# Optimization experiments

Measured on AMD Instinct MI355X. Metric: run time of the kernel, lower is better.

Reference implementation:

```python
import jax, jax.numpy as jnp
import numpy as np

H = 200          # GRU hidden size (hard-coded in module)
D = 300          # embed_dim
V = 50000        # embed_num (vocab)
DOC_TRUNC = 10
N_DOCS = 256
T = 50           # words per sentence


def _p(k, shape):
    return jax.random.normal(k, shape, dtype=jnp.float32) * 0.05


def setup_inputs():
    key = jax.random.key(0)
    ks = jax.random.split(key, 24)
    x = jax.random.randint(ks[0], (N_DOCS * DOC_TRUNC, T), 0, V, dtype=jnp.int32)
    doc_lens = jax.random.randint(ks[1], (N_DOCS,), 0, DOC_TRUNC + 1, dtype=jnp.int32)
    emb = _p(ks[2], (V, D)).at[0].set(0.0)  # padding_idx=0 row is zero
    inp = dict(
        x=x, doc_nums=N_DOCS, doc_lens=doc_lens, emb=emb,
        wf_ih=_p(ks[3], (3 * H, D)), wf_hh=_p(ks[4], (3 * H, H)), wf_bi=_p(ks[5], (3 * H,)), wf_bh=_p(ks[6], (3 * H,)),
        wb_ih=_p(ks[7], (3 * H, D)), wb_hh=_p(ks[8], (3 * H, H)), wb_bi=_p(ks[9], (3 * H,)), wb_bh=_p(ks[10], (3 * H,)),
        sf_ih=_p(ks[11], (3 * H, 2 * H)), sf_hh=_p(ks[12], (3 * H, H)), sf_bi=_p(ks[13], (3 * H,)), sf_bh=_p(ks[14], (3 * H,)),
        sb_ih=_p(ks[15], (3 * H, 2 * H)), sb_hh=_p(ks[16], (3 * H, H)), sb_bi=_p(ks[17], (3 * H,)), sb_bh=_p(ks[18], (3 * H,)),
        doc_w=_p(ks[19], (1, 2 * H)), doc_b=_p(ks[20], (1,)),
        sent_w=_p(ks[21], (DOC_TRUNC, 2 * H)), sent_b=_p(ks[22], (DOC_TRUNC,)),
    )
    return inp


def _gru_dir(xseq, w_ih, w_hh, b_ih, b_hh, reverse=False):
    # xseq: [B, T, Din] -> outputs [B, T, H], torch GRU gate order (r, z, n)
    if reverse:
        xseq = xseq[:, ::-1]
    gx = jnp.einsum('btd,gd->btg', xseq, w_ih) + b_ih  # [B, T, 3H]
    gx = jnp.moveaxis(gx, 1, 0)                        # [T, B, 3H]
    h0 = jnp.zeros((xseq.shape[0], H), xseq.dtype)

    def step(h, gxt):
        gh = h @ w_hh.T + b_hh
        xr, xz, xn = jnp.split(gxt, 3, axis=-1)
        hr, hz, hn = jnp.split(gh, 3, axis=-1)
        r = jax.nn.sigmoid(xr + hr)
        z = jax.nn.sigmoid(xz + hz)
        n = jnp.tanh(xn + r * hn)
        h_new = (1.0 - z) * n + z * h
        return h_new, h_new

    _, hs = jax.lax.scan(step, h0, gx)
    hs = jnp.moveaxis(hs, 0, 1)  # [B, T, H]
    if reverse:
        hs = hs[:, ::-1]
    return hs


def _bigru(xseq, fw, bw):
    return jnp.concatenate([_gru_dir(xseq, *fw), _gru_dir(xseq, *bw, reverse=True)], axis=-1)


def _avg_pool(xseq, lens):
    # Faithful to max_pool1d helper: avg over first lens[i] timesteps, zeros if len==0.
    Tn = xseq.shape[1]
    mask = (jnp.arange(Tn)[None, :] < lens[:, None]).astype(xseq.dtype)  # [B, T]
    s = jnp.einsum('btf,bt->bf', xseq, mask)
    denom = jnp.maximum(lens, 1).astype(xseq.dtype)[:, None]
    return jnp.where((lens == 0)[:, None], jnp.zeros_like(s), s / denom)


def reference(x, doc_nums, doc_lens, emb,
              wf_ih, wf_hh, wf_bi, wf_bh, wb_ih, wb_hh, wb_bi, wb_bh,
              sf_ih, sf_hh, sf_bi, sf_bh, sb_ih, sb_hh, sb_bi, sb_bh,
              doc_w, doc_b, sent_w, sent_b):
    sent_lens = jnp.sum(jnp.sign(x), axis=1)                 # [B_sent]
    e = emb[x]                                               # [B_sent, T, D]
    hw = _bigru(e, (wf_ih, wf_hh, wf_bi, wf_bh), (wb_ih, wb_hh, wb_bi, wb_bh))  # [B_sent, T, 2H]
    s = _avg_pool(hw, sent_lens)                             # [B_sent, 2H]
    s = s.reshape(-1, DOC_TRUNC, 2 * H)                      # [N_docs, doc_trunc, 2H]
    hs = _bigru(s, (sf_ih, sf_hh, sf_bi, sf_bh), (sb_ih, sb_hh, sb_bi, sb_bh))  # [N_docs, doc_trunc, 2H]
    d = _avg_pool(hs, doc_lens)                              # [N_docs, 2H]
    doc_pro = (d @ doc_w.T + doc_b).reshape(-1)              # [N_docs]
    sent_pro = d @ sent_w.T + sent_b                         # [N_docs, doc_trunc]
    dl = np.asarray(doc_lens)                                # concrete index data (static)
    rows = np.repeat(np.arange(dl.shape[0]), dl)
    cols = np.concatenate([np.arange(int(l)) for l in dl]).astype(np.int32) if rows.size else np.zeros((0,), np.int32)
    target = jnp.concatenate([doc_pro, sent_pro[rows, cols]])
    return jax.nn.sigmoid(target)
```

## Files before the change

### kernel.cpp

```cpp
#include <hip/hip_runtime.h>
#include <hip/hip_bf16.h>


typedef __hip_bfloat16 bf16;
typedef _Float16 h16x8 __attribute__((ext_vector_type(8)));
typedef __fp16 fp16x2 __attribute__((ext_vector_type(2)));
typedef float f32x4 __attribute__((ext_vector_type(4)));

#define HDIM 200
#define NS   2560
#define TW   50
#define ND   256
#define DTR  10
#define VEMB 50000

#define GT   13
#define NT   39
#define NTP  40
#define KCH  7
#define HSTR 232
#define KC_W 10
#define KC_S 13

__device__ __forceinline__ float sigf(float x) {
    return __builtin_amdgcn_rcpf(1.f + __expf(-x));
}
__device__ __forceinline__ float tanh_fast(float x) {
    float e = __expf(2.f * x);
    return (e - 1.f) * __builtin_amdgcn_rcpf(e + 1.f);
}
__device__ __forceinline__ unsigned short f2h(float x) {
    union { _Float16 h; unsigned short u; } v;
    v.h = (_Float16)x;
    return v.u;
}
__device__ __forceinline__ float h2f(unsigned short u) {
    union { _Float16 h; unsigned short u; } v;
    v.u = u;
    return (float)v.h;
}
__device__ __forceinline__ unsigned pk2h(float a, float b) {
    union { fp16x2 p; unsigned u; } v;
    v.p = __builtin_amdgcn_cvt_pkrtz(a, b);
    return v.u;
}
__device__ __forceinline__ float hfsel(uint2 v, int rg) {
    unsigned u = (rg & 2) ? v.y : v.x;
    return h2f((unsigned short)((rg & 1) ? (u >> 16) : (u & 0xFFFFu)));
}

#define PB_EMBH 12500
#define PB_WHH  (PB_EMBH + 273)
#define PB_BIH  (PB_WHH + 460)
#define PB_ALL  (PB_BIH + 20)

__global__ void prepack_all(
    const float* __restrict__ emb, unsigned short* __restrict__ embH,
    const float* __restrict__ whh0, const float* __restrict__ whh1,
    const float* __restrict__ whh2, const float* __restrict__ whh3,
    unsigned short* __restrict__ Bhh,
    const float* __restrict__ wih0, const float* __restrict__ wih1,
    const float* __restrict__ wih2, const float* __restrict__ wih3,
    unsigned short* __restrict__ BiW0, unsigned short* __restrict__ BiW1,
    unsigned short* __restrict__ BiS0, unsigned short* __restrict__ BiS1,
    const int* __restrict__ x, int* __restrict__ sl,
    const float* bi0, const float* bh0, const float* bi1, const float* bh1,
    const float* bi2, const float* bh2, const float* bi3, const float* bh3,
    float* __restrict__ bt)
{
    const int b = blockIdx.x;
    const int tid = threadIdx.x;

    if (b < PB_EMBH) {
        int gid = b * 256 + tid;
        int row = gid >> 6, c = gid & 63;
        if (c >= 40) return;
        int k0 = c * 8;
        unsigned short vals[8] __attribute__((aligned(16)));
        if (k0 + 7 < 300) {
            const float4 f0 = *reinterpret_cast<const float4*>(emb + (size_t)row * 300 + k0);
            const float4 f1 = *reinterpret_cast<const float4*>(emb + (size_t)row * 300 + k0 + 4);
            unsigned u0 = pk2h(f0.x, f0.y), u1 = pk2h(f0.z, f0.w);
            unsigned u2 = pk2h(f1.x, f1.y), u3 = pk2h(f1.z, f1.w);
            vals[0] = (unsigned short)u0; vals[1] = (unsigned short)(u0 >> 16);
            vals[2] = (unsigned short)u1; vals[3] = (unsigned short)(u1 >> 16);
            vals[4] = (unsigned short)u2; vals[5] = (unsigned short)(u2 >> 16);
            vals[6] = (unsigned short)u3; vals[7] = (unsigned short)(u3 >> 16);
        } else {
#pragma unroll
            for (int jj = 0; jj < 8; ++jj) {
                int k = k0 + jj;
                vals[jj] = (k < 300) ? f2h(emb[(size_t)row * 300 + k]) : (unsigned short)0;
            }
        }
        *reinterpret_cast<uint4*>(embH + (size_t)row * 320 + k0) =
            *reinterpret_cast<const uint4*>(vals);
        return;
    }

    if (b < PB_WHH) {
        int gid = (b - PB_EMBH) * 256 + tid;
        if (gid >= 4 * NT * KCH * 64) return;
        int lane = gid & 63;
        int f = gid >> 6;
        int kc = f % KCH;
        int tIdx = (f / KCH) % NT;
        int d = f / (KCH * NT);
        const float* w = (d == 0) ? whh0 : (d == 1) ? whh1 : (d == 2) ? whh2 : whh3;
        int g = tIdx / GT, j = tIdx % GT;
        int il = j * 16 + (lane & 15);
        int n = g * HDIM + il;
        int kb = kc * 32 + (lane >> 4) * 8;
        unsigned short vals[8] __attribute__((aligned(16)));
#pragma unroll
        for (int jj = 0; jj < 8; ++jj) {
            int k = kb + jj;
            float v = (il < HDIM && k < HDIM) ? w[n * HDIM + k] : 0.f;
            vals[jj] = f2h(v);
        }
        *reinterpret_cast<float4*>(reinterpret_cast<char*>(Bhh) + (size_t)gid * 16) =
            *reinterpret_cast<const float4*>(vals);
        return;
    }

    if (b < PB_BIH) {
        int rel = b - PB_WHH;
        const float* w; unsigned short* Bp; int Kin, KC, base;
        if (rel < 100)      { w = wih0; Bp = BiW0; Kin = 300; KC = KC_W; base = 0; }
        else if (rel < 200) { w = wih1; Bp = BiW1; Kin = 300; KC = KC_W; base = 100; }
        else if (rel < 330) { w = wih2; Bp = BiS0; Kin = 400; KC = KC_S; base = 200; }
        else                { w = wih3; Bp = BiS1; Kin = 400; KC = KC_S; base = 330; }
        int gid = (rel - base) * 256 + tid;
        if (gid >= NTP * KC * 64) return;
        int lane = gid & 63;
        int f = gid >> 6;
        int kc = f % KC;
        int tIdx = f / KC;
        int g = tIdx / GT, j = tIdx % GT;
        int il = j * 16 + (lane & 15);
        int n = g * HDIM + il;
        int kb = kc * 32 + (lane >> 4) * 8;
        unsigned short vals[8] __attribute__((aligned(16)));
#pragma unroll
        for (int jj = 0; jj < 8; ++jj) {
            int k = kb + jj;
            float v = (tIdx < NT && il < HDIM && k < Kin) ? w[n * Kin + k] : 0.f;
            vals[jj] = f2h(v);
        }
        *reinterpret_cast<float4*>(reinterpret_cast<char*>(Bp) + (size_t)gid * 16) =
            *reinterpret_cast<const float4*>(vals);
        return;
    }

    {
        int gid = (b - PB_BIH) * 256 + tid;
        if (gid < NS) {
            int c = 0;
            for (int t = 0; t < TW; ++t) c += (x[gid * TW + t] != 0) ? 1 : 0;
            sl[gid] = c;
            return;
        }
        int g2 = gid - NS;
        if (g2 >= 4 * 624) return;
        int d = g2 / 624, col = g2 % 624;
        int g = col / 208, i = col % 208;
        const float* bi = (d == 0) ? bi0 : (d == 1) ? bi1 : (d == 2) ? bi2 : bi3;
        const float* bh = (d == 0) ? bh0 : (d == 1) ? bh1 : (d == 2) ? bh2 : bh3;
        float v = 0.f;
        if (i < HDIM) v = (g < 2) ? (bi[g * HDIM + i] + bh[g * HDIM + i]) : bi[2 * HDIM + i];
        bt[g2] = v;
    }
}

__global__ __launch_bounds__(512, 4) void gemm_word(
    const unsigned short* __restrict__ embH, const int* __restrict__ idx,
    const unsigned short* __restrict__ Bp,
    const float* __restrict__ bt, unsigned short* __restrict__ gxOut)
{
    __shared__ __align__(16) unsigned short As[64 * 320];

    const int tid = threadIdx.x;
    const int n_w = tid >> 6, lane = tid & 63;
    const int bm = blockIdx.x;

    {
        const int srow = tid >> 3, q8 = tid & 7;
        int rp = bm * 64 + srow;
        int tok = idx[(rp % NS) * TW + (rp / NS)];
        const unsigned short* src = embH + (size_t)tok * 320;
        const int rx = srow & 7;
        unsigned short* dst = &As[srow * 320];
#pragma unroll
        for (int jj = 0; jj < 5; ++jj) {
            int c = q8 + jj * 8;
            uint4 v = *reinterpret_cast<const uint4*>(src + c * 8);
            int slot = c ^ rx;
            *reinterpret_cast<uint4*>(dst + slot * 8) = v;
        }
    }
    __syncthreads();

    f32x4 acc[4][5];
#pragma unroll
    for (int i = 0; i < 4; ++i)
#pragma unroll
        for (int j = 0; j < 5; ++j) acc[i][j] = (f32x4){0.f, 0.f, 0.f, 0.f};

    const uint4* bq = reinterpret_cast<const uint4*>(Bp);
    const int q = lane >> 4, r15 = lane & 15;
    const int sx = r15 & 7;

#pragma unroll 2
    for (int kc = 0; kc < KC_W; ++kc) {
        h16x8 ah[4];
        const int slot = (kc * 4 + q) ^ sx;
#pragma unroll
        for (int mt = 0; mt < 4; ++mt)
            ah[mt] = *reinterpret_cast<const h16x8*>(
                &As[(mt * 16 + r15) * 320 + slot * 8]);
        uint4 b[5];
#pragma unroll
        for (int j = 0; j < 5; ++j) {
            int gnt = n_w * 5 + j;
            b[j] = bq[(size_t)(gnt * KC_W + kc) * 64 + lane];
        }
#pragma unroll
        for (int mt = 0; mt < 4; ++mt)
#pragma unroll
            for (int j = 0; j < 5; ++j)
                acc[mt][j] = __builtin_amdgcn_mfma_f32_16x16x32_f16(
                    ah[mt], *reinterpret_cast<const h16x8*>(&b[j]),
                    acc[mt][j], 0, 0, 0);
    }

    float btv[5];
#pragma unroll
    for (int j = 0; j < 5; ++j) {
        int gnt = n_w * 5 + j;
        btv[j] = (gnt < NT) ? bt[gnt * 16 + r15] : 0.f;
    }

#pragma unroll
    for (int mt = 0; mt < 4; ++mt) {
        int gmt = bm * 4 + mt;
#pragma unroll
        for (int j = 0; j < 5; ++j) {
            int gnt = n_w * 5 + j;
            if (gnt < NT) {
                uint2 v;
                v.x = pk2h(acc[mt][j][0] + btv[j], acc[mt][j][1] + btv[j]);
                v.y = pk2h(acc[mt][j][2] + btv[j], acc[mt][j][3] + btv[j]);
                *reinterpret_cast<uint2*>(reinterpret_cast<char*>(gxOut) +
                    ((size_t)(gmt * NT + gnt) * 64 + lane) * 8) = v;
            }
        }
    }
}

__global__ __launch_bounds__(512, 2) void gemm_sent(
    const float* __restrict__ Afl, int astride,
    const unsigned short* __restrict__ Bp0, const unsigned short* __restrict__ Bp1,
    const float* __restrict__ bt0, const float* __restrict__ bt1,
    unsigned short* __restrict__ gx0, unsigned short* __restrict__ gx1, int nF)
{
    __shared__ __align__(16) unsigned short As[2][128 * 32];

    const int tid = threadIdx.x;
    const int wv = tid >> 6, lane = tid & 63;
    const int d = (blockIdx.x >= nF) ? 1 : 0;
    const int bm = d ? (blockIdx.x - nF) : blockIdx.x;
    const unsigned short* Bp = d ? Bp1 : Bp0;
    const float* bt = d ? bt1 : bt0;
    unsigned short* gxOut = d ? gx1 : gx0;
    const int m_w = wv & 1, n_w = wv >> 1;

    int aaddr[4];
#pragma unroll
    for (int mt = 0; mt < 4; ++mt) {
        int row = m_w * 64 + mt * 16 + (lane & 15);
        aaddr[mt] = row * 32 + (((lane >> 4) ^ ((row >> 1) & 3)) << 3);
    }

    const int srow = tid >> 2, qk = tid & 3;
    const int ssw = (srow >> 1) & 3;

    f32x4 acc[4][10];
#pragma unroll
    for (int i = 0; i < 4; ++i)
#pragma unroll
        for (int j = 0; j < 10; ++j) acc[i][j] = (f32x4){0.f, 0.f, 0.f, 0.f};

    const uint4* bq = reinterpret_cast<const uint4*>(Bp);
    const float* arow = Afl + (size_t)(bm * 128 + srow) * astride + qk * 8;

    float4 f[2], fn[2];
#pragma unroll
    for (int j = 0; j < 2; ++j)
        f[j] = *reinterpret_cast<const float4*>(arow + j * 4);

    for (int kc = 0; kc < KC_S; ++kc) {
        unsigned short* Ab = &As[kc & 1][0];
        {
            uint4 vh;
            vh.x = pk2h(f[0].x, f[0].y);
            vh.y = pk2h(f[0].z, f[0].w);
            vh.z = pk2h(f[1].x, f[1].y);
            vh.w = pk2h(f[1].z, f[1].w);
            int slot = qk ^ ssw;
            *reinterpret_cast<uint4*>(&Ab[srow * 32 + slot * 8]) = vh;
        }
        __syncthreads();

        if (kc + 1 < KC_S) {
#pragma unroll
            for (int j = 0; j < 2; ++j)
                fn[j] = *reinterpret_cast<const float4*>(arow + (kc + 1) * 32 + j * 4);
        }

        h16x8 ah[4];
#pragma unroll
        for (int mt = 0; mt < 4; ++mt)
            ah[mt] = *reinterpret_cast<const h16x8*>(&Ab[aaddr[mt]]);

#pragma unroll
        for (int half = 0; half < 2; ++half) {
            uint4 b[5];
#pragma unroll
            for (int j = 0; j < 5; ++j) {
                int gnt = n_w * 10 + half * 5 + j;
                b[j] = bq[(size_t)(gnt * KC_S + kc) * 64 + lane];
            }
#pragma unroll
            for (int mt = 0; mt < 4; ++mt)
#pragma unroll
                for (int j = 0; j < 5; ++j)
                    acc[mt][half * 5 + j] = __builtin_amdgcn_mfma_f32_16x16x32_f16(
                        ah[mt], *reinterpret_cast<const h16x8*>(&b[j]),
                        acc[mt][half * 5 + j], 0, 0, 0);
        }
        if (kc + 1 < KC_S) { f[0] = fn[0]; f[1] = fn[1]; }
    }

    float btv[10];
#pragma unroll
    for (int j = 0; j < 10; ++j) {
        int gnt = n_w * 10 + j;
        btv[j] = (gnt < NT) ? bt[gnt * 16 + (lane & 15)] : 0.f;
    }

#pragma unroll
    for (int mt = 0; mt < 4; ++mt) {
        int gmt = bm * 8 + m_w * 4 + mt;
#pragma unroll
        for (int j = 0; j < 10; ++j) {
            int gnt = n_w * 10 + j;
            if (gnt < NT) {
                uint2 v;
                v.x = pk2h(acc[mt][j][0] + btv[j], acc[mt][j][1] + btv[j]);
                v.y = pk2h(acc[mt][j][2] + btv[j], acc[mt][j][3] + btv[j]);
                *reinterpret_cast<uint2*>(reinterpret_cast<char*>(gxOut) +
                    ((size_t)(gmt * NT + gnt) * 64 + lane) * 8) = v;
            }
        }
    }
}

__global__ __launch_bounds__(448, 2) void gru_word(
    const unsigned short* __restrict__ gxA, const unsigned short* __restrict__ gxB,
    const unsigned short* __restrict__ Bp, int dirBase0, int dirBase1,
    const float* __restrict__ bh0, const float* __restrict__ bh1,
    const int* __restrict__ lens, float* __restrict__ pool,
    int S, int T, int poolMode, int nF)
{
    __shared__ __align__(16) unsigned short hh[2][16 * HSTR];

    const int dsel = (blockIdx.x >= nF) ? 1 : 0;
    const int lb = dsel ? (blockIdx.x - nF) : blockIdx.x;
    const unsigned short* gx = dsel ? gxB : gxA;
    const int dirBase = dsel ? dirBase1 : dirBase0;
    const float* bh = dsel ? bh1 : bh0;
    const int dirOff = dsel ? HDIM : 0;
    const int rev = dsel;

    const int tid = threadIdx.x;
    const int w = tid >> 6, lane = tid & 63;
    const int quad = lane >> 4, c = lane & 15;
    const int row0 = lb * 16;
    const int j0 = 2 * w, j1 = 2 * w + 1;
    const int i0 = j0 * 16 + c, i1 = j1 * 16 + c;
    const bool t1v = (j1 < GT);
    const bool iv0 = (i0 < HDIM), iv1 = t1v && (i1 < HDIM);

    for (int p = tid; p < 2 * 16 * HSTR; p += 448)
        hh[0][p] = 0;
    __syncthreads();

    const float bhn0 = iv0 ? bh[2 * HDIM + i0] : 0.f;
    const float bhn1 = iv1 ? bh[2 * HDIM + i1] : 0.f;

    int slen[4];
    float hr0[4], hr1[4], pa0[4], pa1[4];
#pragma unroll
    for (int rg = 0; rg < 4; ++rg) {
        int L = lens[row0 + quad * 4 + rg];
        if (L < 0) L = 0;
        if (L > T) L = T;
        slen[rg] = L;
        hr0[rg] = 0.f; hr1[rg] = 0.f; pa0[rg] = 0.f; pa1[rg] = 0.f;
    }

    const float4* Bq = reinterpret_cast<const float4*>(Bp);
    h16x8 bfr[2][3][KCH];
#pragma unroll
    for (int g = 0; g < 3; ++g)
#pragma unroll
        for (int kc = 0; kc < KCH; ++kc) {
            {
                int fidx = (dirBase + g * GT + j0) * KCH + kc;
                float4 raw = Bq[(size_t)fidx * 64 + lane];
                bfr[0][g][kc] = *reinterpret_cast<h16x8*>(&raw);
            }
            if (t1v) {
                int fidx = (dirBase + g * GT + j1) * KCH + kc;
                float4 raw = Bq[(size_t)fidx * 64 + lane];
                bfr[1][g][kc] = *reinterpret_cast<h16x8*>(&raw);
            }
        }

    const char* gxb = reinterpret_cast<const char*>(gx);
    const int am = c * HSTR + quad * 8;
    const int SG = S >> 4;
    const int hw0 = (quad * 4) * HSTR + i0;
    const int hw1 = (quad * 4) * HSTR + i1;
    const int dstep = (rev ? -SG : SG) * NT * 512;
    int boff;
    {
        const int t0 = rev ? (T - 1) : 0;
        boff = ((t0 * SG + lb) * NT) * 512 + lane * 8;
    }
    __syncthreads();

    for (int ts = 0; ts < T; ++ts) {
        const int t = rev ? (T - 1 - ts) : ts;
        const int cur = ts & 1, nxt = cur ^ 1;

        uint2 gx0[3], gx1[3];
#pragma unroll
        for (int g = 0; g < 3; ++g) {
            gx0[g] = *reinterpret_cast<const uint2*>(gxb + boff + (g * GT + j0) * 512);
            if (t1v)
                gx1[g] = *reinterpret_cast<const uint2*>(gxb + boff + (g * GT + j1) * 512);
        }
        boff += dstep;

        f32x4 a00 = (f32x4){0.f, 0.f, 0.f, 0.f}, a01 = a00, a02 = a00;
        f32x4 a10 = a00, a11 = a00, a12 = a00;
#pragma unroll
        for (int kc = 0; kc < KCH; ++kc) {
            h16x8 ah = *reinterpret_cast<const h16x8*>(&hh[cur][am + kc * 32]);
            a00 = __builtin_amdgcn_mfma_f32_16x16x32_f16(ah, bfr[0][0][kc], a00, 0, 0, 0);
            a01 = __builtin_amdgcn_mfma_f32_16x16x32_f16(ah, bfr[0][1][kc], a01, 0, 0, 0);
            a02 = __builtin_amdgcn_mfma_f32_16x16x32_f16(ah, bfr[0][2][kc], a02, 0, 0, 0);
            if (t1v) {
                a10 = __builtin_amdgcn_mfma_f32_16x16x32_f16(ah, bfr[1][0][kc], a10, 0, 0, 0);
                a11 = __builtin_amdgcn_mfma_f32_16x16x32_f16(ah, bfr[1][1][kc], a11, 0, 0, 0);
                a12 = __builtin_amdgcn_mfma_f32_16x16x32_f16(ah, bfr[1][2][kc], a12, 0, 0, 0);
            }
        }

        if (iv0) {
#pragma unroll
            for (int rg = 0; rg < 4; ++rg) {
                float r = sigf(hfsel(gx0[0], rg) + a00[rg]);
                float z = sigf(hfsel(gx0[1], rg) + a01[rg]);
                float n = tanh_fast(hfsel(gx0[2], rg) + r * (a02[rg] + bhn0));
                float hnew = n + z * (hr0[rg] - n);
                hr0[rg] = hnew;
                hh[nxt][hw0 + rg * HSTR] = f2h(hnew);
                pa0[rg] += (t < slen[rg]) ? hnew : 0.f;
            }
        }
        if (iv1) {
#pragma unroll
            for (int rg = 0; rg < 4; ++rg) {
                float r = sigf(hfsel(gx1[0], rg) + a10[rg]);
                float z = sigf(hfsel(gx1[1], rg) + a11[rg]);
                float n = tanh_fast(hfsel(gx1[2], rg) + r * (a12[rg] + bhn1));
                float hnew = n + z * (hr1[rg] - n);
                hr1[rg] = hnew;
                hh[nxt][hw1 + rg * HSTR] = f2h(hnew);
                pa1[rg] += (t < slen[rg]) ? hnew : 0.f;
            }
        }
        __syncthreads();
    }

#pragma unroll
    for (int rg = 0; rg < 4; ++rg) {
        int sg = row0 + quad * 4 + rg;
        int L = slen[rg];
        int prow = poolMode ? ((sg % 10) * ND + sg / 10) : sg;
        float inv = (L > 0) ? 1.f / (float)L : 0.f;
        if (iv0) pool[(size_t)prow * 400 + dirOff + i0] = pa0[rg] * inv;
        if (iv1) pool[(size_t)prow * 400 + dirOff + i1] = pa1[rg] * inv;
    }
}

__global__ __launch_bounds__(832, 4) void gru_fused(
    const unsigned short* __restrict__ gxA, const unsigned short* __restrict__ gxB,
    const unsigned short* __restrict__ Bp, int dirBase0, int dirBase1,
    const float* __restrict__ bh0, const float* __restrict__ bh1,
    const int* __restrict__ lens, float* __restrict__ pool,
    int S, int T, int poolMode, int nF)
{
    __shared__ __align__(16) unsigned short hh[2][16 * HSTR];

    const int dsel = (blockIdx.x >= nF) ? 1 : 0;
    const int lb = dsel ? (blockIdx.x - nF) : blockIdx.x;
    const unsigned short* gx = dsel ? gxB : gxA;
    const int dirBase = dsel ? dirBase1 : dirBase0;
    const float* bh = dsel ? bh1 : bh0;
    const int dirOff = dsel ? HDIM : 0;
    const int rev = dsel;

    const int tid = threadIdx.x;
    const int w = tid >> 6, lane = tid & 63;
    const int quad = lane >> 4, c = lane & 15;
    const int row0 = lb * 16;
    const int i = w * 16 + c;
    const bool iv = (i < HDIM);

    for (int p = tid; p < 16 * HSTR; p += 832) { hh[0][p] = 0; hh[1][p] = 0; }
    __syncthreads();

    const float bhn = iv ? bh[2 * HDIM + i] : 0.f;

    int slen[4];
    float hreg[4], pacc[4];
#pragma unroll
    for (int rg = 0; rg < 4; ++rg) {
        int L = lens[row0 + quad * 4 + rg];
        if (L < 0) L = 0;
        if (L > T) L = T;
        slen[rg] = L;
        hreg[rg] = 0.f; pacc[rg] = 0.f;
    }

    const float4* Bq = reinterpret_cast<const float4*>(Bp);
    h16x8 bfr[3][7];
#pragma unroll
    for (int g = 0; g < 3; ++g)
#pragma unroll
        for (int kc = 0; kc < KCH; ++kc) {
            int fidx = (dirBase + g * GT + w) * KCH + kc;
            float4 raw = Bq[(size_t)fidx * 64 + lane];
            bfr[g][kc] = *reinterpret_cast<h16x8*>(&raw);
        }

    const char* gxb = reinterpret_cast<const char*>(gx);
    const int am = c * HSTR + quad * 8;
    const int SG = S >> 4;
    const int hw0 = (quad * 4) * HSTR + i;
    const int GSTR = GT * 64 * 8;
    const int dstep = (rev ? -SG : SG) * NT * 512;
    __syncthreads();

    uint2 gxv[3], gnx[3];
    int boff;
    {
        const int t0 = rev ? (T - 1) : 0;
        boff = (((t0 * SG + lb) * NT + w) * 64 + lane) * 8;
#pragma unroll
        for (int g = 0; g < 3; ++g)
            gxv[g] = *reinterpret_cast<const uint2*>(gxb + boff + g * GSTR);
        boff += dstep;
    }

    for (int ts = 0; ts < T; ++ts) {
        const int t = rev ? (T - 1 - ts) : ts;
        const int cur = ts & 1, nxt = cur ^ 1;

        if (ts + 1 < T) {
#pragma unroll
            for (int g = 0; g < 3; ++g)
                gnx[g] = *reinterpret_cast<const uint2*>(gxb + boff + g * GSTR);
            boff += dstep;
        }

        f32x4 a0 = (f32x4){0.f, 0.f, 0.f, 0.f}, a1 = a0, a2 = a0;
#pragma unroll
        for (int kc = 0; kc < KCH; ++kc) {
            h16x8 ah = *reinterpret_cast<const h16x8*>(&hh[cur][am + kc * 32]);
            a0 = __builtin_amdgcn_mfma_f32_16x16x32_f16(ah, bfr[0][kc], a0, 0, 0, 0);
            a1 = __builtin_amdgcn_mfma_f32_16x16x32_f16(ah, bfr[1][kc], a1, 0, 0, 0);
            a2 = __builtin_amdgcn_mfma_f32_16x16x32_f16(ah, bfr[2][kc], a2, 0, 0, 0);
        }

        if (iv) {
#pragma unroll
            for (int rg = 0; rg < 4; ++rg) {
                float xr = hfsel(gxv[0], rg);
                float xz = hfsel(gxv[1], rg);
                float xn = hfsel(gxv[2], rg);
                float r = sigf(xr + a0[rg]);
                float z = sigf(xz + a1[rg]);
                float n = tanh_fast(xn + r * (a2[rg] + bhn));
                float hnew = n + z * (hreg[rg] - n);
                hreg[rg] = hnew;
                hh[nxt][hw0 + rg * HSTR] = f2h(hnew);
                pacc[rg] += (t < slen[rg]) ? hnew : 0.f;
            }
        }
        __syncthreads();
        if (ts + 1 < T) {
#pragma unroll
            for (int g = 0; g < 3; ++g) gxv[g] = gnx[g];
        }
    }

    if (iv) {
#pragma unroll
        for (int rg = 0; rg < 4; ++rg) {
            int sg = row0 + quad * 4 + rg;
            int L = slen[rg];
            float v = (L > 0) ? pacc[rg] / (float)L : 0.f;
            int prow = poolMode ? ((sg % 10) * ND + sg / 10) : sg;
            pool[(size_t)prow * 400 + dirOff + i] = v;
        }
    }
}

__global__ __launch_bounds__(64) void head_kernel(
    const float* __restrict__ d_pool, const int* __restrict__ doc_lens,
    const float* __restrict__ doc_w, const float* __restrict__ doc_b,
    const float* __restrict__ sent_w, const float* __restrict__ sent_b,
    float* __restrict__ out)
{
    const int d = blockIdx.x;
    const int lane = threadIdx.x;

    int part = 0;
#pragma unroll
    for (int rep = 0; rep < 4; ++rep) {
        int j = lane + rep * 64;
        int v = doc_lens[j];
        v = (v < 0) ? 0 : (v > DTR ? DTR : v);
        if (j < d) part += v;
    }
#pragma unroll
    for (int off = 32; off; off >>= 1) part += __shfl_down(part, off);
    int soff = __shfl(part, 0);

    int dl = doc_lens[d];
    dl = (dl < 0) ? 0 : (dl > DTR ? DTR : dl);
    const float* dv = d_pool + (size_t)d * 400;

    for (int o = 0; o <= dl; ++o) {
        const float* wrow = (o == 0) ? doc_w : sent_w + (o - 1) * 400;
        float s = 0.f;
        for (int f = lane; f < 400; f += 64) s += dv[f] * wrow[f];
#pragma unroll
        for (int off = 32; off; off >>= 1) s += __shfl_down(s, off);
        if (lane == 0) {
            float bias = (o == 0) ? doc_b[0] : sent_b[o - 1];
            out[(o == 0) ? d : (ND + soff + (o - 1))] = sigf(s + bias);
        }
    }
}

extern "C" void kernel_launch(void* const* d_in, const int* in_sizes, int n_in,
                              void* d_out, int out_size, void* d_ws, size_t ws_size,
                              hipStream_t stream) {
    const int*   x        = (const int*)d_in[0];
    const int*   doc_lens = (const int*)d_in[2];
    const float* emb      = (const float*)d_in[3];
    const float* wf_ih = (const float*)d_in[4];
    const float* wf_hh = (const float*)d_in[5];
    const float* wf_bi = (const float*)d_in[6];
    const float* wf_bh = (const float*)d_in[7];
    const float* wb_ih = (const float*)d_in[8];
    const float* wb_hh = (const float*)d_in[9];
    const float* wb_bi = (const float*)d_in[10];
    const float* wb_bh = (const float*)d_in[11];
    const float* sf_ih = (const float*)d_in[12];
    const float* sf_hh = (const float*)d_in[13];
    const float* sf_bi = (const float*)d_in[14];
    const float* sf_bh = (const float*)d_in[15];
    const float* sb_ih = (const float*)d_in[16];
    const float* sb_hh = (const float*)d_in[17];
    const float* sb_bi = (const float*)d_in[18];
    const float* sb_bh = (const float*)d_in[19];
    const float* doc_w  = (const float*)d_in[20];
    const float* doc_b  = (const float*)d_in[21];
    const float* sent_w = (const float*)d_in[22];
    const float* sent_b = (const float*)d_in[23];

    const size_t GXSZ = 159744000;
    char* ws = (char*)d_ws;
    const size_t base = GXSZ;

    unsigned short* gxF  = (unsigned short*)(ws);
    unsigned short* gxS0 = (unsigned short*)(ws);
    unsigned short* gxS1 = (unsigned short*)(ws + 8000000);
    float* s_in   = (float*)(ws + base);
    float* dpool  = (float*)(ws + base + 4096256);
    int*   sl     = (int*)(ws + base + 4096256 + 409600);
    unsigned short* Bhh  = (unsigned short*)(ws + base + 4096256 + 409600 + 10240);
    unsigned short* BiW0 = (unsigned short*)((char*)Bhh + 1118208);
    unsigned short* BiW1 = BiW0 + NTP * KC_W * 64 * 8;
    unsigned short* BiS0 = (unsigned short*)((char*)BiW0 + 819200);
    unsigned short* BiS1 = BiS0 + NTP * KC_S * 64 * 8;
    float* bt     = (float*)((char*)BiS0 + 1064960);
    unsigned short* embH = (unsigned short*)((char*)bt + 9984);

    prepack_all<<<PB_ALL, 256, 0, stream>>>(
        emb, embH,
        wf_hh, wb_hh, sf_hh, sb_hh, Bhh,
        wf_ih, wb_ih, sf_ih, sb_ih, BiW0, BiW1, BiS0, BiS1,
        x, sl,
        wf_bi, wf_bh, wb_bi, wb_bh, sf_bi, sf_bh, sb_bi, sb_bh, bt);

    gemm_word<<<2000, 512, 0, stream>>>(embH, x, BiW0, bt + 0, gxF);
    gru_word<<<160, 448, 0, stream>>>(
        gxF, gxF, Bhh, 0 * NT, 1 * NT, wf_bh, wb_bh, sl, s_in, NS, TW, 1, 160);
    gemm_word<<<2000, 512, 0, stream>>>(embH, x, BiW1, bt + 624, gxF);
    gru_word<<<160, 448, 0, stream>>>(
        gxF, gxF, Bhh, 0 * NT, 1 * NT, wf_bh, wb_bh, sl, s_in, NS, TW, 1, 0);

    gemm_sent<<<40, 512, 0, stream>>>(
        s_in, 400, BiS0, BiS1, bt + 2 * 624, bt + 3 * 624, gxS0, gxS1, 20);
    gru_fused<<<32, 832, 0, stream>>>(
        gxS0, gxS1, Bhh, 2 * NT, 3 * NT, sf_bh, sb_bh, doc_lens, dpool, ND, DTR, 0, 16);

    head_kernel<<<ND, 64, 0, stream>>>(dpool, doc_lens, doc_w, doc_b, sent_w, sent_b, (float*)d_out);
}
```

Measured before the change: 551.5 us.

## Prefetch GRU gate inputs into LDS asynchronously and reverse first GEMM block order

```diff
diff --git a/kernel.cpp b/kernel.cpp
--- a/kernel.cpp
+++ b/kernel.cpp
@@ -21,6 +21,9 @@
 #define HSTR 232
 #define KC_W 10
 #define KC_S 13
+
+typedef const __attribute__((address_space(1))) unsigned gbl_u32;
+typedef __attribute__((address_space(3))) unsigned lds_u32;
 
 __device__ __forceinline__ float sigf(float x) {
     return __builtin_amdgcn_rcpf(1.f + __expf(-x));
@@ -175,13 +178,13 @@
 __global__ __launch_bounds__(512, 4) void gemm_word(
     const unsigned short* __restrict__ embH, const int* __restrict__ idx,
     const unsigned short* __restrict__ Bp,
-    const float* __restrict__ bt, unsigned short* __restrict__ gxOut)
+    const float* __restrict__ bt, unsigned short* __restrict__ gxOut, int revOrd)
 {
     __shared__ __align__(16) unsigned short As[64 * 320];
 
     const int tid = threadIdx.x;
     const int n_w = tid >> 6, lane = tid & 63;
-    const int bm = blockIdx.x;
+    const int bm = revOrd ? (gridDim.x - 1 - blockIdx.x) : blockIdx.x;
 
     {
         const int srow = tid >> 3, q8 = tid & 7;
@@ -373,6 +376,7 @@
     int S, int T, int poolMode, int nF)
 {
     __shared__ __align__(16) unsigned short hh[2][16 * HSTR];
+    __shared__ __align__(16) unsigned short gxs[2][7][3][512];
 
     const int dsel = (blockIdx.x >= nF) ? 1 : 0;
     const int lb = dsel ? (blockIdx.x - nF) : blockIdx.x;
@@ -393,7 +397,6 @@
 
     for (int p = tid; p < 2 * 16 * HSTR; p += 448)
         hh[0][p] = 0;
-    __syncthreads();
 
     const float bhn0 = iv0 ? bh[2 * HDIM + i0] : 0.f;
     const float bhn1 = iv1 ? bh[2 * HDIM + i1] : 0.f;
@@ -436,7 +439,17 @@
     int boff;
     {
         const int t0 = rev ? (T - 1) : 0;
-        boff = ((t0 * SG + lb) * NT) * 512 + lane * 8;
+        boff = ((t0 * SG + lb) * NT) * 512;
+    }
+
+    {
+        const char* src0 = gxb + boff;
+#pragma unroll
+        for (int g = 0; g < 3; ++g)
+            __builtin_amdgcn_global_load_lds(
+                (gbl_u32*)(src0 + (g * GT + j0) * 512 + lane * 16),
+                (lds_u32*)(&gxs[0][w][g][0]), 16, 0, 0);
+        boff += dstep;
     }
     __syncthreads();
 
@@ -444,14 +457,15 @@
         const int t = rev ? (T - 1 - ts) : ts;
         const int cur = ts & 1, nxt = cur ^ 1;
 
-        uint2 gx0[3], gx1[3];
-#pragma unroll
-        for (int g = 0; g < 3; ++g) {
-            gx0[g] = *reinterpret_cast<const uint2*>(gxb + boff + (g * GT + j0) * 512);
-            if (t1v)
-                gx1[g] = *reinterpret_cast<const uint2*>(gxb + boff + (g * GT + j1) * 512);
-        }
-        boff += dstep;
+        if (ts + 1 < T) {
+            const char* srcn = gxb + boff;
+#pragma unroll
+            for (int g = 0; g < 3; ++g)
+                __builtin_amdgcn_global_load_lds(
+                    (gbl_u32*)(srcn + (g * GT + j0) * 512 + lane * 16),
+                    (lds_u32*)(&gxs[nxt][w][g][0]), 16, 0, 0);
+            boff += dstep;
+        }
 
         f32x4 a00 = (f32x4){0.f, 0.f, 0.f, 0.f}, a01 = a00, a02 = a00;
         f32x4 a10 = a00, a11 = a00, a12 = a00;
@@ -466,6 +480,14 @@
                 a11 = __builtin_amdgcn_mfma_f32_16x16x32_f16(ah, bfr[1][1][kc], a11, 0, 0, 0);
                 a12 = __builtin_amdgcn_mfma_f32_16x16x32_f16(ah, bfr[1][2][kc], a12, 0, 0, 0);
             }
+        }
+
+        uint2 gx0[3], gx1[3];
+#pragma unroll
+        for (int g = 0; g < 3; ++g) {
+            gx0[g] = *reinterpret_cast<const uint2*>(&gxs[cur][w][g][lane * 4]);
+            if (t1v)
+                gx1[g] = *reinterpret_cast<const uint2*>(&gxs[cur][w][g][256 + lane * 4]);
         }
 
         if (iv0) {
@@ -720,10 +742,10 @@
         x, sl,
         wf_bi, wf_bh, wb_bi, wb_bh, sf_bi, sf_bh, sb_bi, sb_bh, bt);
 
-    gemm_word<<<2000, 512, 0, stream>>>(embH, x, BiW0, bt + 0, gxF);
+    gemm_word<<<2000, 512, 0, stream>>>(embH, x, BiW0, bt + 0, gxF, 1);
     gru_word<<<160, 448, 0, stream>>>(
         gxF, gxF, Bhh, 0 * NT, 1 * NT, wf_bh, wb_bh, sl, s_in, NS, TW, 1, 160);
-    gemm_word<<<2000, 512, 0, stream>>>(embH, x, BiW1, bt + 624, gxF);
+    gemm_word<<<2000, 512, 0, stream>>>(embH, x, BiW1, bt + 624, gxF, 0);
     gru_word<<<160, 448, 0, stream>>>(
         gxF, gxF, Bhh, 0 * NT, 1 * NT, wf_bh, wb_bh, sl, s_in, NS, TW, 1, 0);
 
```

Measured after the change: 549.5 us. About the same (-0.4%).
